# Kernel tuning notes

Measured on AMD Instinct MI355X. Metric: run time of the kernel, lower is better.

## Reference

```python
import jax, jax.numpy as jnp
import numpy as np

VOCAB, EMBED, HIDDEN = 32000, 512, 1024
B, T = 64, 512


def setup_inputs() -> dict:
    key = jax.random.key(0)
    ks = jax.random.split(key, 8)
    s = 0.02
    return {
        "x": jax.random.randint(ks[0], (B, T), 0, VOCAB, dtype=jnp.int32),
        "emb_table": jax.random.normal(ks[1], (VOCAB, EMBED), jnp.float32) * s,
        "W_ih": jax.random.normal(ks[2], (4 * HIDDEN, EMBED), jnp.float32) * s,
        "W_hh": jax.random.normal(ks[3], (4 * HIDDEN, HIDDEN), jnp.float32) * s,
        "b_ih": jax.random.normal(ks[4], (4 * HIDDEN,), jnp.float32) * s,
        "b_hh": jax.random.normal(ks[5], (4 * HIDDEN,), jnp.float32) * s,
        "W_fc": jax.random.normal(ks[6], (VOCAB, HIDDEN), jnp.float32) * s,
        "b_fc": jax.random.normal(ks[7], (VOCAB,), jnp.float32) * s,
    }


def _lstm(emb, W_ih, W_hh, b_ih, b_hh):
    # emb: [B, T, E]. Precompute input projections for all timesteps (one big GEMM).
    xp = jnp.einsum("bte,ge->btg", emb, W_ih) + b_ih + b_hh  # [B, T, 4H]
    xp = jnp.swapaxes(xp, 0, 1)  # [T, B, 4H] for scan over time
    H = W_hh.shape[1]
    h0 = jnp.zeros((emb.shape[0], H), emb.dtype)
    c0 = jnp.zeros((emb.shape[0], H), emb.dtype)

    def step(carry, xp_t):
        h, c = carry
        g = xp_t + h @ W_hh.T  # [B, 4H]
        i, f, gg, o = jnp.split(g, 4, axis=-1)  # PyTorch gate order: i, f, g, o
        i = jax.nn.sigmoid(i)
        f = jax.nn.sigmoid(f)
        gg = jnp.tanh(gg)
        o = jax.nn.sigmoid(o)
        c = f * c + i * gg
        h = o * jnp.tanh(c)
        return (h, c), None

    (h_last, _), _ = jax.lax.scan(step, (h0, c0), xp)
    return h_last  # [B, H] == out[:, -1, :]


def reference(x, emb_table, W_ih, W_hh, b_ih, b_hh, W_fc, b_fc):
    emb = emb_table[x]  # [B, T, E]
    h_last = _lstm(emb, W_ih, W_hh, b_ih, b_hh)
    return h_last @ W_fc.T + b_fc  # [B, VOCAB]
```

## Files before the change

kernel.cpp:

```cpp
#include <hip/hip_runtime.h>

typedef unsigned short u16;
typedef float f32x4 __attribute__((ext_vector_type(4)));
typedef _Float16 f16x8 __attribute__((ext_vector_type(8)));

#define VOCAB 32000
#define EMBED 512
#define HIDDEN 1024
#define BATCH 64
#define SEQ 512
#define G4H 4096
#define LBLK 64

static __device__ __forceinline__ float h2f(u16 v) {
  _Float16 h;
  __builtin_memcpy(&h, &v, 2);
  return (float)h;
}
static __device__ __forceinline__ u16 f2h(float f) {
  _Float16 h = (_Float16)f;
  u16 v;
  __builtin_memcpy(&v, &h, 2);
  return v;
}
static __device__ __forceinline__ float sigmoidf_(float x) {
  return 1.f / (1.f + __expf(-x));
}
static __device__ __forceinline__ f16x8 cvt8(const float* p) {
  float4 a = *(const float4*)p, b = *(const float4*)(p + 4);
  f16x8 v;
  v[0] = (_Float16)a.x; v[1] = (_Float16)a.y;
  v[2] = (_Float16)a.z; v[3] = (_Float16)a.w;
  v[4] = (_Float16)b.x; v[5] = (_Float16)b.y;
  v[6] = (_Float16)b.z; v[7] = (_Float16)b.w;
  return v;
}

#define GLOADC(dst, addr)                                  \
  asm volatile("global_load_dwordx4 %0, %1, off sc0 sc1"  \
               : "=v"(dst)                                 \
               : "v"(addr)                                 \
               : "memory")

__global__ __launch_bounds__(256, 2) void phaseA(
    const int* __restrict__ x, const float* __restrict__ emb,
    const float* __restrict__ Wih, const float* __restrict__ bih,
    const float* __restrict__ bhh, u16* __restrict__ xp) {
  __shared__ __align__(16) _Float16 Al[128 * 32];
  __shared__ __align__(16) _Float16 Bl[128 * 32];
  const int t = threadIdx.x;
  const int bx = blockIdx.x;
  const int by = blockIdx.y;
  const int m0 = by * 128;
  const int u0 = bx * 32;

  const int r0 = x[m0 + (t >> 2)];
  const int r1 = x[m0 + 64 + (t >> 2)];
  const int nl0 = t >> 2, nl1 = 64 + (t >> 2);
  const int wrow0 = u0 + (nl0 >> 2) + (nl0 & 3) * 1024;
  const int wrow1 = u0 + (nl1 >> 2) + (nl1 & 3) * 1024;
  const int kq = t & 3;

  const int wid = t >> 6, l = t & 63;
  const int wr = wid >> 1, wc = wid & 1;
  const int lm = l & 15, lk = l >> 4;

  f32x4 acc[4][4];
#pragma unroll
  for (int i = 0; i < 4; ++i)
#pragma unroll
    for (int j = 0; j < 4; ++j) acc[i][j] = (f32x4){0.f, 0.f, 0.f, 0.f};

  for (int k0 = 0; k0 < EMBED; k0 += 32) {
    *(f16x8*)(Al + t * 8) = cvt8(emb + (size_t)r0 * EMBED + k0 + kq * 8);
    *(f16x8*)(Al + (t + 256) * 8) = cvt8(emb + (size_t)r1 * EMBED + k0 + kq * 8);
    *(f16x8*)(Bl + t * 8) = cvt8(Wih + (size_t)wrow0 * EMBED + k0 + kq * 8);
    *(f16x8*)(Bl + (t + 256) * 8) = cvt8(Wih + (size_t)wrow1 * EMBED + k0 + kq * 8);
    __syncthreads();
    f16x8 af[4], bf[4];
#pragma unroll
    for (int mt = 0; mt < 4; ++mt)
      af[mt] = *(const f16x8*)(Al + (wr * 64 + mt * 16 + lm) * 32 + lk * 8);
#pragma unroll
    for (int nt = 0; nt < 4; ++nt)
      bf[nt] = *(const f16x8*)(Bl + (wc * 64 + nt * 16 + lm) * 32 + lk * 8);
#pragma unroll
    for (int mt = 0; mt < 4; ++mt)
#pragma unroll
      for (int nt = 0; nt < 4; ++nt)
        acc[mt][nt] = __builtin_amdgcn_mfma_f32_16x16x32_f16(
            af[mt], bf[nt], acc[mt][nt], 0, 0, 0);
    __syncthreads();
  }

#pragma unroll
  for (int nt = 0; nt < 4; ++nt) {
    const int nloc = wc * 64 + nt * 16 + lm;
    const int grow = u0 + (nloc >> 2) + (nloc & 3) * 1024;
    const float bsum = bih[grow] + bhh[grow];
#pragma unroll
    for (int mt = 0; mt < 4; ++mt)
#pragma unroll
      for (int r = 0; r < 4; ++r) {
        const int m = m0 + wr * 64 + mt * 16 + lk * 4 + r;
        const int bb = m >> 9, tt = m & 511;
        xp[((size_t)tt * 64 + bb) * G4H + bx * 128 + nloc] =
            f2h(acc[mt][nt][r] + bsum);
      }
  }
}

__global__ __launch_bounds__(512, 2) void lstm_steps(
    const u16* __restrict__ xp, const float* __restrict__ Whh,
    u16* __restrict__ hA, u16* __restrict__ hB, unsigned* __restrict__ flags) {
  __shared__ __align__(16) u16 ps[64 * 64 * 8];
  char* psb = (char*)ps;
  const int t = threadIdx.x;
  const int blk = blockIdx.x;
  const int kw = t >> 6;
  const int l = t & 63;
  const int lm = l & 15, lk = l >> 4;

  f16x8 wf[4][4];
#pragma unroll
  for (int rt = 0; rt < 4; ++rt)
#pragma unroll
    for (int kf = 0; kf < 4; ++kf)
      wf[rt][kf] = cvt8(Whh + (size_t)(rt * HIDDEN + blk * 16 + lm) * HIDDEN +
                        kw * 128 + kf * 32 + lk * 8);

  const int gb = t >> 3, gup = t & 7;
  float c0 = 0.f, c1 = 0.f;

  for (int s = 0; s < SEQ; ++s) {
    const u16* hp = (s & 1) ? hB : hA;
    u16* hn = (s & 1) ? hA : hB;

    f16x8 xv;
    GLOADC(xv, xp + (size_t)s * (64 * G4H) + (size_t)gb * G4H + blk * 64 + gup * 8);

    f16x8 bv[2][4];
#pragma unroll
    for (int kf = 0; kf < 4; ++kf)
      GLOADC(bv[0][kf], hp + (size_t)lm * HIDDEN + kw * 128 + kf * 32 + lk * 8);

    f32x4 acc[4][4];
#pragma unroll
    for (int i = 0; i < 4; ++i)
#pragma unroll
      for (int j = 0; j < 4; ++j) acc[i][j] = (f32x4){0.f, 0.f, 0.f, 0.f};

#pragma unroll
    for (int bt = 0; bt < 4; ++bt) {
      const int cur = bt & 1;
      if (bt < 3) {
        const int nxt = cur ^ 1;
#pragma unroll
        for (int kf = 0; kf < 4; ++kf)
          GLOADC(bv[nxt][kf], hp + (size_t)((bt + 1) * 16 + lm) * HIDDEN +
                                  kw * 128 + kf * 32 + lk * 8);
        asm volatile("s_waitcnt vmcnt(4)" ::: "memory");
      } else {
        asm volatile("s_waitcnt vmcnt(0)" ::: "memory");
      }
      __builtin_amdgcn_sched_barrier(0);
#pragma unroll
      for (int rt = 0; rt < 4; ++rt)
#pragma unroll
        for (int kf = 0; kf < 4; ++kf)
          acc[rt][bt] = __builtin_amdgcn_mfma_f32_16x16x32_f16(
              wf[rt][kf], bv[cur][kf], acc[rt][bt], 0, 0, 0);
    }

#pragma unroll
    for (int rt = 0; rt < 4; ++rt)
#pragma unroll
      for (int bt = 0; bt < 4; ++bt)
#pragma unroll
        for (int r = 0; r < 4; ++r) {
          const int row = rt * 16 + lk * 4 + r;
          const int bb = bt * 16 + lm;
          const unsigned off =
              (unsigned)(row * 1024 + bb * 16 + kw * 2) ^
              (unsigned)((row & 7) << 4);
          *(u16*)(psb + off) = f2h(acc[rt][bt][r]);
        }
    __syncthreads();

    float go0, go1;
    {
      const int u0 = gup * 2;
      float gg0[4], gg1[4];
#pragma unroll
      for (int c = 0; c < 4; ++c) {
        const int row0 = c * 16 + u0;
        const unsigned o0 = (unsigned)(row0 * 1024 + gb * 16) ^
                            (unsigned)((row0 & 7) << 4);
        const f16x8 p0 = *(const f16x8*)(psb + o0);
        const int row1 = row0 + 1;
        const unsigned o1 = (unsigned)(row1 * 1024 + gb * 16) ^
                            (unsigned)((row1 & 7) << 4);
        const f16x8 p1 = *(const f16x8*)(psb + o1);
        gg0[c] = ((float)p0[0] + (float)p0[1]) + ((float)p0[2] + (float)p0[3]) +
                 ((float)p0[4] + (float)p0[5]) + ((float)p0[6] + (float)p0[7]) +
                 (float)xv[c];
        gg1[c] = ((float)p1[0] + (float)p1[1]) + ((float)p1[2] + (float)p1[3]) +
                 ((float)p1[4] + (float)p1[5]) + ((float)p1[6] + (float)p1[7]) +
                 (float)xv[4 + c];
      }
      {
        const float ig = sigmoidf_(gg0[0]), fg = sigmoidf_(gg0[1]);
        const float gv = tanhf(gg0[2]), og = sigmoidf_(gg0[3]);
        c0 = fg * c0 + ig * gv;
        go0 = og * tanhf(c0);
      }
      {
        const float ig = sigmoidf_(gg1[0]), fg = sigmoidf_(gg1[1]);
        const float gv = tanhf(gg1[2]), og = sigmoidf_(gg1[3]);
        c1 = fg * c1 + ig * gv;
        go1 = og * tanhf(c1);
      }
    }
    const unsigned hpack = (unsigned)f2h(go0) | ((unsigned)f2h(go1) << 16);
    __hip_atomic_store(
        (unsigned*)(hn + (size_t)gb * HIDDEN + blk * 16 + gup * 2), hpack,
        __ATOMIC_RELAXED, __HIP_MEMORY_SCOPE_AGENT);

    if (s == SEQ - 1) break;

    asm volatile("s_waitcnt vmcnt(0)" ::: "memory");
    __syncthreads();
    if (t == 0)
      __hip_atomic_store(flags + blk * 32, (unsigned)(s + 1), __ATOMIC_RELAXED,
                         __HIP_MEMORY_SCOPE_AGENT);
    if (t < LBLK) {
      const unsigned tgt = (unsigned)(s + 1);
      while (true) {
        unsigned v = __hip_atomic_load(flags + t * 32, __ATOMIC_RELAXED,
                                       __HIP_MEMORY_SCOPE_AGENT);
        if (__all((int)(v >= tgt))) break;
        __builtin_amdgcn_s_sleep(1);
      }
    }
    __syncthreads();
  }
}

__global__ __launch_bounds__(256) void transpose_h(const u16* __restrict__ h,
                                                   u16* __restrict__ hT) {
  const int e = blockIdx.x * 256 + threadIdx.x;
  hT[e] = h[(size_t)(e & 63) * HIDDEN + (e >> 6)];
}

__global__ __launch_bounds__(256) void phaseC(
    const u16* __restrict__ hT, const float* __restrict__ Wfc,
    const float* __restrict__ bfc, float* __restrict__ out) {
  __shared__ float Ws[32][129];
  __shared__ __align__(16) float hs[128][68];
  const int t = threadIdx.x;
  const int v0 = blockIdx.x * 32;
  const int lane = t & 63;
  const int w = t >> 6;
  const int v = lane & 31;
  const int bbase = ((w << 1) | (lane >> 5)) << 3;
  float acc[8] = {0.f, 0.f, 0.f, 0.f, 0.f, 0.f, 0.f, 0.f};

  for (int kc = 0; kc < HIDDEN; kc += 128) {
#pragma unroll
    for (int i = 0; i < 16; ++i) {
      int e = t + i * 256;
      Ws[e >> 7][e & 127] =
          Wfc[(size_t)(v0 + (e >> 7)) * HIDDEN + kc + (e & 127)];
    }
#pragma unroll
    for (int i = 0; i < 8; ++i) {
      int e = t + i * 256;
      int k = e >> 4, b4 = e & 15;
      ushort4 hv = *(const ushort4*)&hT[(size_t)(kc + k) * 64 + b4 * 4];
      float4 fv = {h2f(hv.x), h2f(hv.y), h2f(hv.z), h2f(hv.w)};
      *(float4*)&hs[k][b4 * 4] = fv;
    }
    __syncthreads();
    for (int k = 0; k < 128; ++k) {
      const float wv = Ws[v][k];
      const float4 ha = *(const float4*)&hs[k][bbase];
      const float4 hb = *(const float4*)&hs[k][bbase + 4];
      acc[0] = fmaf(wv, ha.x, acc[0]);
      acc[1] = fmaf(wv, ha.y, acc[1]);
      acc[2] = fmaf(wv, ha.z, acc[2]);
      acc[3] = fmaf(wv, ha.w, acc[3]);
      acc[4] = fmaf(wv, hb.x, acc[4]);
      acc[5] = fmaf(wv, hb.y, acc[5]);
      acc[6] = fmaf(wv, hb.z, acc[6]);
      acc[7] = fmaf(wv, hb.w, acc[7]);
    }
    __syncthreads();
  }
  const float bias = bfc[v0 + v];
#pragma unroll
  for (int i = 0; i < 8; ++i)
    out[(size_t)(bbase + i) * VOCAB + v0 + v] = acc[i] + bias;
}

extern "C" void kernel_launch(void* const* d_in, const int* in_sizes, int n_in,
                              void* d_out, int out_size, void* d_ws,
                              size_t ws_size, hipStream_t stream) {
  const int* x = (const int*)d_in[0];
  const float* emb = (const float*)d_in[1];
  const float* Wih = (const float*)d_in[2];
  const float* Whh = (const float*)d_in[3];
  const float* bih = (const float*)d_in[4];
  const float* bhh = (const float*)d_in[5];
  const float* Wfc = (const float*)d_in[6];
  const float* bfc = (const float*)d_in[7];
  float* out = (float*)d_out;

  char* ws = (char*)d_ws;
  const size_t XPB = (size_t)SEQ * 64 * G4H * sizeof(u16);
  u16* xp = (u16*)ws;
  u16* hA = (u16*)(ws + XPB);
  u16* hB = (u16*)(ws + XPB + 131072);
  u16* hT = (u16*)(ws + XPB + 262144);
  unsigned* flags = (unsigned*)(ws + XPB + 393216);

  hipMemsetAsync(hA, 0, 131072, stream);
  hipMemsetAsync(flags, 0, LBLK * 128, stream);

  phaseA<<<dim3(32, 256), 256, 0, stream>>>(x, emb, Wih, bih, bhh, xp);

  {
    const u16* xp_c = xp;
    const float* Whh_c = Whh;
    void* args[] = {(void*)&xp_c, (void*)&Whh_c, (void*)&hA, (void*)&hB,
                    (void*)&flags};
    hipLaunchCooperativeKernel((const void*)lstm_steps, dim3(LBLK), dim3(512),
                               args, 0, stream);
  }

  transpose_h<<<256, 256, 0, stream>>>((const u16*)hA, hT);
  phaseC<<<1000, 256, 0, stream>>>(hT, Wfc, bfc, out);
}
```

Measured before the change: 4.248 ms.

## Issue all h loads upfront, vectorize partial-sum LDS layout, fuse final transpose

The recurrent step now issues all 16 hidden-state loads at once and staggers waits, instead of double-buffering them. The LDS partial-sum layout is reorganized so each wave writes packed 8-byte chunks, and the reducers read one 32-bit word per k-slice. tanhf is replaced by an exp-based formula. The last step writes h directly in transposed layout, which removes the separate transpose kernel. All of this targets per-step latency in the serial recurrence, at the cost of more registers and more LDS read instructions.

After: 4.312 ms. About the same (+1.5%).

```diff
diff --git a/kernel.cpp b/kernel.cpp
--- a/kernel.cpp
+++ b/kernel.cpp
@@ -1,6 +1,7 @@
 #include <hip/hip_runtime.h>
 
 typedef unsigned short u16;
+typedef unsigned int u32;
 typedef float f32x4 __attribute__((ext_vector_type(4)));
 typedef _Float16 f16x8 __attribute__((ext_vector_type(8)));
 
@@ -23,8 +24,14 @@
   __builtin_memcpy(&v, &h, 2);
   return v;
 }
+static __device__ __forceinline__ u32 pk2h(float a, float b) {
+  return (u32)f2h(a) | ((u32)f2h(b) << 16);
+}
 static __device__ __forceinline__ float sigmoidf_(float x) {
   return 1.f / (1.f + __expf(-x));
+}
+static __device__ __forceinline__ float tanhf_(float x) {
+  return 1.f - 2.f / (__expf(2.f * x) + 1.f);
 }
 static __device__ __forceinline__ f16x8 cvt8(const float* p) {
   float4 a = *(const float4*)p, b = *(const float4*)(p + 4);
@@ -112,9 +119,9 @@
 
 __global__ __launch_bounds__(512, 2) void lstm_steps(
     const u16* __restrict__ xp, const float* __restrict__ Whh,
-    u16* __restrict__ hA, u16* __restrict__ hB, unsigned* __restrict__ flags) {
-  __shared__ __align__(16) u16 ps[64 * 64 * 8];
-  char* psb = (char*)ps;
+    u16* __restrict__ hA, u16* __restrict__ hB, u16* __restrict__ hT,
+    unsigned* __restrict__ flags) {
+  __shared__ __align__(16) char psb[65536];
   const int t = threadIdx.x;
   const int blk = blockIdx.x;
   const int kw = t >> 6;
@@ -130,6 +137,10 @@
                         kw * 128 + kf * 32 + lk * 8);
 
   const int gb = t >> 3, gup = t & 7;
+  const unsigned wbase = (unsigned)(kw * 8192 + l * 8);
+  const unsigned roff = (unsigned)((gb >> 4) * 512 + (gup >> 1) * 128 +
+                                   (gb & 15) * 8 + (gup & 1) * 4);
+  const size_t xpofs = (size_t)gb * G4H + (size_t)blk * 64 + gup * 8;
   float c0 = 0.f, c1 = 0.f;
 
   for (int s = 0; s < SEQ; ++s) {
@@ -137,12 +148,14 @@
     u16* hn = (s & 1) ? hA : hB;
 
     f16x8 xv;
-    GLOADC(xv, xp + (size_t)s * (64 * G4H) + (size_t)gb * G4H + blk * 64 + gup * 8);
-
-    f16x8 bv[2][4];
-#pragma unroll
-    for (int kf = 0; kf < 4; ++kf)
-      GLOADC(bv[0][kf], hp + (size_t)lm * HIDDEN + kw * 128 + kf * 32 + lk * 8);
+    GLOADC(xv, xp + (size_t)s * (64 * G4H) + xpofs);
+    f16x8 bv[4][4];
+#pragma unroll
+    for (int bt = 0; bt < 4; ++bt)
+#pragma unroll
+      for (int kf = 0; kf < 4; ++kf)
+        GLOADC(bv[bt][kf], hp + (size_t)(bt * 16 + lm) * HIDDEN + kw * 128 +
+                               kf * 32 + lk * 8);
 
     f32x4 acc[4][4];
 #pragma unroll
@@ -152,81 +165,68 @@
 
 #pragma unroll
     for (int bt = 0; bt < 4; ++bt) {
-      const int cur = bt & 1;
-      if (bt < 3) {
-        const int nxt = cur ^ 1;
-#pragma unroll
-        for (int kf = 0; kf < 4; ++kf)
-          GLOADC(bv[nxt][kf], hp + (size_t)((bt + 1) * 16 + lm) * HIDDEN +
-                                  kw * 128 + kf * 32 + lk * 8);
-        asm volatile("s_waitcnt vmcnt(4)" ::: "memory");
-      } else {
-        asm volatile("s_waitcnt vmcnt(0)" ::: "memory");
-      }
+      if (bt == 0) asm volatile("s_waitcnt vmcnt(12)" ::: "memory");
+      else if (bt == 1) asm volatile("s_waitcnt vmcnt(8)" ::: "memory");
+      else if (bt == 2) asm volatile("s_waitcnt vmcnt(4)" ::: "memory");
+      else asm volatile("s_waitcnt vmcnt(0)" ::: "memory");
       __builtin_amdgcn_sched_barrier(0);
 #pragma unroll
       for (int rt = 0; rt < 4; ++rt)
 #pragma unroll
         for (int kf = 0; kf < 4; ++kf)
           acc[rt][bt] = __builtin_amdgcn_mfma_f32_16x16x32_f16(
-              wf[rt][kf], bv[cur][kf], acc[rt][bt], 0, 0, 0);
+              wf[rt][kf], bv[bt][kf], acc[rt][bt], 0, 0, 0);
     }
 
 #pragma unroll
     for (int rt = 0; rt < 4; ++rt)
 #pragma unroll
-      for (int bt = 0; bt < 4; ++bt)
-#pragma unroll
-        for (int r = 0; r < 4; ++r) {
-          const int row = rt * 16 + lk * 4 + r;
-          const int bb = bt * 16 + lm;
-          const unsigned off =
-              (unsigned)(row * 1024 + bb * 16 + kw * 2) ^
-              (unsigned)((row & 7) << 4);
-          *(u16*)(psb + off) = f2h(acc[rt][bt][r]);
-        }
-    __syncthreads();
-
+      for (int bt = 0; bt < 4; ++bt) {
+        uint2 v;
+        v.x = pk2h(acc[rt][bt][0], acc[rt][bt][1]);
+        v.y = pk2h(acc[rt][bt][2], acc[rt][bt][3]);
+        *(uint2*)(psb + wbase + (rt * 4 + bt) * 512) = v;
+      }
+    __syncthreads();
+
+    float s0[4], s1[4];
+#pragma unroll
+    for (int c = 0; c < 4; ++c) {
+      s0[c] = (float)xv[c];
+      s1[c] = (float)xv[4 + c];
+    }
+#pragma unroll
+    for (int c = 0; c < 4; ++c)
+#pragma unroll
+      for (int k8 = 0; k8 < 8; ++k8) {
+        const u32 pv = *(const u32*)(psb + k8 * 8192 + c * 2048 + roff);
+        s0[c] += h2f((u16)(pv & 0xffffu));
+        s1[c] += h2f((u16)(pv >> 16));
+      }
     float go0, go1;
     {
-      const int u0 = gup * 2;
-      float gg0[4], gg1[4];
-#pragma unroll
-      for (int c = 0; c < 4; ++c) {
-        const int row0 = c * 16 + u0;
-        const unsigned o0 = (unsigned)(row0 * 1024 + gb * 16) ^
-                            (unsigned)((row0 & 7) << 4);
-        const f16x8 p0 = *(const f16x8*)(psb + o0);
-        const int row1 = row0 + 1;
-        const unsigned o1 = (unsigned)(row1 * 1024 + gb * 16) ^
-                            (unsigned)((row1 & 7) << 4);
-        const f16x8 p1 = *(const f16x8*)(psb + o1);
-        gg0[c] = ((float)p0[0] + (float)p0[1]) + ((float)p0[2] + (float)p0[3]) +
-                 ((float)p0[4] + (float)p0[5]) + ((float)p0[6] + (float)p0[7]) +
-                 (float)xv[c];
-        gg1[c] = ((float)p1[0] + (float)p1[1]) + ((float)p1[2] + (float)p1[3]) +
-                 ((float)p1[4] + (float)p1[5]) + ((float)p1[6] + (float)p1[7]) +
-                 (float)xv[4 + c];
-      }
-      {
-        const float ig = sigmoidf_(gg0[0]), fg = sigmoidf_(gg0[1]);
-        const float gv = tanhf(gg0[2]), og = sigmoidf_(gg0[3]);
-        c0 = fg * c0 + ig * gv;
-        go0 = og * tanhf(c0);
-      }
-      {
-        const float ig = sigmoidf_(gg1[0]), fg = sigmoidf_(gg1[1]);
-        const float gv = tanhf(gg1[2]), og = sigmoidf_(gg1[3]);
-        c1 = fg * c1 + ig * gv;
-        go1 = og * tanhf(c1);
-      }
-    }
+      const float ig = sigmoidf_(s0[0]), fg = sigmoidf_(s0[1]);
+      const float gv = tanhf_(s0[2]), og = sigmoidf_(s0[3]);
+      c0 = fg * c0 + ig * gv;
+      go0 = og * tanhf_(c0);
+    }
+    {
+      const float ig = sigmoidf_(s1[0]), fg = sigmoidf_(s1[1]);
+      const float gv = tanhf_(s1[2]), og = sigmoidf_(s1[3]);
+      c1 = fg * c1 + ig * gv;
+      go1 = og * tanhf_(c1);
+    }
+
+    if (s == SEQ - 1) {
+      hT[(size_t)(blk * 16 + gup * 2) * 64 + gb] = f2h(go0);
+      hT[(size_t)(blk * 16 + gup * 2 + 1) * 64 + gb] = f2h(go1);
+      break;
+    }
+
     const unsigned hpack = (unsigned)f2h(go0) | ((unsigned)f2h(go1) << 16);
     __hip_atomic_store(
         (unsigned*)(hn + (size_t)gb * HIDDEN + blk * 16 + gup * 2), hpack,
         __ATOMIC_RELAXED, __HIP_MEMORY_SCOPE_AGENT);
-
-    if (s == SEQ - 1) break;
 
     asm volatile("s_waitcnt vmcnt(0)" ::: "memory");
     __syncthreads();
@@ -244,12 +244,6 @@
     }
     __syncthreads();
   }
-}
-
-__global__ __launch_bounds__(256) void transpose_h(const u16* __restrict__ h,
-                                                   u16* __restrict__ hT) {
-  const int e = blockIdx.x * 256 + threadIdx.x;
-  hT[e] = h[(size_t)(e & 63) * HIDDEN + (e >> 6)];
 }
 
 __global__ __launch_bounds__(256) void phaseC(
@@ -332,11 +326,10 @@
     const u16* xp_c = xp;
     const float* Whh_c = Whh;
     void* args[] = {(void*)&xp_c, (void*)&Whh_c, (void*)&hA, (void*)&hB,
-                    (void*)&flags};
+                    (void*)&hT,   (void*)&flags};
     hipLaunchCooperativeKernel((const void*)lstm_steps, dim3(LBLK), dim3(512),
                                args, 0, stream);
   }
 
-  transpose_h<<<256, 256, 0, stream>>>((const u16*)hA, hT);
   phaseC<<<1000, 256, 0, stream>>>(hT, Wfc, bfc, out);
 }
```
